# Kernel tuning notes

Measured on AMD Instinct MI355X. Metric: run time of the kernel, lower is better.

Reference implementation:

```python
import jax, jax.numpy as jnp
import numpy as np
from jax.scipy.special import gammaln

EPS = 1e-8
N_SAMPLES = 2 ** 17
ATTACK_FULL_SIZE = 2048
CPD = 16
N_RES = 16
EXPR = 2
N_OSC = 2
N_GAUSS = 8
N_EVENTS = 4
FRAMES = 128
DEF_FRAMES = 128
N_LEVELS = 11  # log2(ATTACK_FULL_SIZE)


def unit_norm(x, axis=-1):
    return x / (jnp.linalg.norm(x, axis=axis, keepdims=True) + EPS)


def fft_convolve(a, b):
    # zero-pad to 2n to avoid circular wraparound, multiply spectra, crop to n
    n = a.shape[-1]
    fa = jnp.fft.rfft(a, n=2 * n, axis=-1)
    fb = jnp.fft.rfft(b, n=2 * n, axis=-1)
    return jnp.fft.irfft(fa * fb, n=2 * n, axis=-1)[..., :n]


def upsample_with_holes(x, size):
    # zero-insertion upsampling: place frames at stride `factor`
    factor = size // x.shape[-1]
    out = jnp.zeros(x.shape[:-1] + (size,), x.dtype)
    return out.at[..., ::factor].set(x)


def interpolate_last_axis(x, size):
    # linear interpolation, align_corners=False semantics (torch F.interpolate)
    n = x.shape[-1]
    scale = n / size
    src = jnp.clip((jnp.arange(size) + 0.5) * scale - 0.5, 0.0, n - 1.0)
    lo = jnp.floor(src).astype(jnp.int32)
    hi = jnp.minimum(lo + 1, n - 1)
    w = (src - lo).astype(x.dtype)
    return x[..., lo] * (1.0 - w) + x[..., hi] * w


def ensure_last_axis_length(x, size):
    n = x.shape[-1]
    if n == size:
        return x
    if n > size:
        return x[..., :size]
    return jnp.pad(x, [(0, 0)] * (x.ndim - 1) + [(0, size - n)])


def sparse_softmax(x):
    # hard one-hot forward, softmax straight-through backward
    sm = jax.nn.softmax(x, axis=-1)
    hard = jax.nn.one_hot(jnp.argmax(x, axis=-1), x.shape[-1], dtype=x.dtype)
    return hard + sm - jax.lax.stop_gradient(sm)


def hierarchical_dirac(p):
    # p: (..., L, 2) binary choices per level -> one-hot dirac of length 2**L
    sel = sparse_softmax(p)
    sig = sel[..., 0, :]
    for i in range(1, p.shape[-2]):
        sig = (sig[..., :, None] * sel[..., i, :][..., None, :]).reshape(*sig.shape[:-1], -1)
    return sig


def gamma_pdf(mean, std, n_elements):
    # gamma pdf on support (eps, 1], parameterized by mean/std
    t = jnp.linspace(EPS, 1.0, n_elements)
    k = (mean / (std + EPS)) ** 2
    rate = mean / (std ** 2 + EPS)
    k = k[..., None]
    rate = rate[..., None]
    logp = k * jnp.log(rate + EPS) + (k - 1.0) * jnp.log(t) - rate * t - gammaln(k)
    return jnp.exp(logp)


def damped_harmonic_oscillator(time, mass, damping, tension, x0):
    # underdamped closed-form solution, v0 = 0
    omega0_sq = tension / mass
    gamma = damping / (2.0 * mass)
    omega = jnp.sqrt(omega0_sq - gamma ** 2)
    A = x0
    B = gamma * x0 / omega
    return jnp.exp(-gamma * time) * (A * jnp.cos(omega * time) + B * jnp.sin(omega * time))


def dho_block(damping, mass, tension, disp, amps, tmod=None, scaling=None):
    time = jnp.linspace(0.0, 10.0, N_SAMPLES).reshape(1, 1, 1, N_SAMPLES)
    t = tension[..., None]  # (N_OSC, N_RES, EXPR, 1)
    if tmod is not None:
        t = t + tmod[0] * scaling  # broadcast -> (N_OSC, N_RES, EXPR, N_SAMPLES)
    x = damped_harmonic_oscillator(
        time,
        jax.nn.sigmoid(mass[..., None]) * 2.0,
        jax.nn.sigmoid(damping[..., None]) * 30.0,
        10.0 ** t,
        disp[..., None],
    )
    x = (x * amps).sum(axis=0)  # sum over oscillators
    return x.reshape(1, 1, N_RES, EXPR, N_SAMPLES)


def attack_envelopes(means, stds, amps, pos, overall_amp):
    m, s, a = jnp.abs(means), jnp.abs(stds), jnp.abs(amps)
    p = hierarchical_dirac(pos)  # (1,1,CPD,NG,2048)
    x = gamma_pdf(m, s, ATTACK_FULL_SIZE) * a[..., None]
    x = fft_convolve(x, p)
    x = x.sum(axis=2)  # (1,1,NG,2048)
    x = unit_norm(x)
    x = x * overall_amp[..., None]  # broadcast -> (1,1,CPD,NG,2048)
    x = x.sum(axis=-2)  # (1,1,CPD,2048)
    return x.reshape(CPD, ATTACK_FULL_SIZE)


def _forward(control_signal, deformations, ae_means, ae_stds, ae_amps, ae_pos,
             ae_overall_amp, dho_damping, dho_mass, dho_tension, dho_disp, dho_amp,
             influences, stack_mix, router, layer_mix, gains, attack_noise):
    b, ne, cpd, frames = control_signal.shape
    # --- DampedHarmonicOscillatorStack ---
    o1 = dho_block(dho_damping[0], dho_mass[0], dho_tension[0], dho_disp[0], dho_amp[0])
    o2 = dho_block(dho_damping[1], dho_mass[1], dho_tension[1], dho_disp[1], dho_amp[1], o1, influences[0])
    o3 = dho_block(dho_damping[2], dho_mass[2], dho_tension[2], dho_disp[2], dho_amp[2], o2, influences[1])
    res = (jnp.stack([o1, o2, o3], axis=-1) * jax.nn.softmax(stack_mix, axis=-1)).sum(axis=-1)
    res = unit_norm(res)
    # --- AttackEnvelopes ---
    ae = attack_envelopes(ae_means, ae_stds, ae_amps, ae_pos, ae_overall_amp)
    # --- execute_layer ---
    routed = jnp.einsum('becf,cr->berf', control_signal, router)
    before = routed
    res = unit_norm(res)  # execute_layer normalizes again
    routed = upsample_with_holes(routed.reshape(b, ne, N_RES, 1, frames), N_SAMPLES)
    # ae.shape[-1] == window_size, so materialize_attack_envelopes just multiplies noise
    impulse = ensure_last_axis_length(ae * attack_noise, N_SAMPLES).reshape(1, 1, cpd, 1, N_SAMPLES)
    routed = fft_convolve(impulse, routed)  # (1,ne,N_RES,1,S)
    cs = routed.reshape(1, ne, cpd, N_SAMPLES).sum(axis=1, keepdims=True)
    conv = fft_convolve(routed, res)  # (1,ne,N_RES,EXPR,S)
    base = jnp.zeros_like(deformations).at[:, :, 0:1, :].set(1.0)
    d = jax.nn.softmax(base + deformations, axis=-2)
    d = interpolate_last_axis(d.reshape(b, 1, 1, EXPR, -1), N_SAMPLES)
    x = (d * conv).sum(axis=-2)  # (1,ne,N_RES,S)
    mixes = jax.nn.softmax(layer_mix.reshape(1, 1, N_RES, 1, 1, 2), axis=-1)
    stacked = jnp.stack([routed, x.reshape(routed.shape)], axis=-1)
    x = (mixes * stacked).sum(axis=-1)
    x = x.reshape(1, 1, N_RES, -1)
    summed = jnp.tanh(x * jnp.abs(gains.reshape(1, 1, N_RES, 1)))
    summed = summed.sum(axis=-2, keepdims=True)
    return summed, before, cs


def setup_inputs() -> dict:
    key = jax.random.key(0)
    ks = jax.random.split(key, 20)
    u = lambda k, shape, lo, hi: jax.random.uniform(k, shape, jnp.float32, lo, hi)
    inp = {}
    inp['control_signal'] = jax.random.uniform(ks[0], (1, N_EVENTS, CPD, FRAMES), jnp.float32)
    inp['deformations'] = jax.random.normal(ks[1], (1, 1, EXPR, DEF_FRAMES), jnp.float32)
    inp['ae_means'] = u(ks[2], (1, 1, CPD, N_GAUSS), -6.0, 6.0)
    inp['ae_stds'] = u(ks[3], (1, 1, CPD, N_GAUSS), 0.5, 6.0)
    inp['ae_amps'] = u(ks[4], (1, 1, CPD, N_GAUSS), -6.0, 6.0)
    inp['ae_pos'] = u(ks[5], (1, 1, CPD, N_GAUSS, N_LEVELS, 2), -1.0, 1.0)
    inp['ae_overall_amp'] = u(ks[6], (1, 1, CPD, 1), -1.0, 1.0)
    inp['dho_damping'] = u(ks[7], (3, N_OSC, N_RES, EXPR), 0.5, 1.5)
    inp['dho_mass'] = u(ks[8], (3, N_OSC, N_RES, EXPR), -2.0, 2.0)
    inp['dho_tension'] = u(ks[9], (3, N_OSC, N_RES, EXPR), 4.0, 9.0)
    inp['dho_disp'] = u(ks[10], (3, N_OSC, N_RES, EXPR), -1.0, 2.0)
    inp['dho_amp'] = u(ks[11], (3, N_OSC, N_RES, EXPR, 1), -1.0, 1.0)
    inp['influences'] = u(ks[12], (2, N_OSC, N_RES, EXPR, 1), -0.01, 0.01)
    inp['stack_mix'] = u(ks[13], (1, 1, N_RES, EXPR, 1, 3), -1.0, 1.0)
    router = u(ks[14], (CPD, N_RES), -1.0, 1.0)
    mask = (jax.random.uniform(ks[15], (CPD, N_RES)) < 0.1).astype(jnp.float32)
    inp['router'] = router * mask
    inp['layer_mix'] = u(ks[16], (N_RES, 2), -1.0, 1.0)
    inp['gains'] = u(ks[17], (N_RES, 1), 0.01, 1.1)
    inp['attack_noise'] = u(ks[18], (CPD, ATTACK_FULL_SIZE), -1.0, 1.0)
    return inp


def reference(control_signal, deformations, ae_means, ae_stds, ae_amps, ae_pos,
              ae_overall_amp, dho_damping, dho_mass, dho_tension, dho_disp, dho_amp,
              influences, stack_mix, router, layer_mix, gains, attack_noise):
    return _forward(control_signal, deformations, ae_means, ae_stds, ae_amps, ae_pos,
                    ae_overall_amp, dho_damping, dho_mass, dho_tension, dho_disp, dho_amp,
                    influences, stack_mix, router, layer_mix, gains, attack_noise)
```

## Files before the change

kernel.cpp:

```cpp
#include <hip/hip_runtime.h>
#include <math.h>

#define NS 131072
#define EPSF 1e-8f

#define OFF_IMP    8388608u
#define OFF_VG     8421376u
#define OFF_DW     8437760u
#define OFF_FV     8568832u
#define OFF_NORM   8577024u
#define OFF_MIX0   8577064u
#define OFF_MIX1   8577080u
#define OFF_GABS   8577096u
#define OFF_PART   8578560u
#define OFF_GSSP   8594944u
#define OFF_DHP    8595200u

#define AFRAG_USH  4194304u
#define ABF2_USH   4726784u
#define HB_USH     8388608u

typedef __attribute__((ext_vector_type(8))) short short8;
typedef __attribute__((ext_vector_type(4))) float floatx4;
typedef __attribute__((ext_vector_type(4))) unsigned short ushort4v;

#define INV2PI 0.15915494309189535f

__device__ __forceinline__ float sigmf(float x) { return 1.0f / (1.0f + expf(-x)); }

__device__ __forceinline__ unsigned short f2bf(float x) {
  unsigned u = __float_as_uint(x);
  unsigned r = (u + 0x7FFFu + ((u >> 16) & 1u)) >> 16;
  return (unsigned short)r;
}

__global__ __launch_bounds__(256) void k0_params(
    const float* __restrict__ ddmp, const float* __restrict__ dmas,
    const float* __restrict__ dten, const float* __restrict__ ddisp,
    const float* __restrict__ damp, const float* __restrict__ infl,
    const float* __restrict__ smix, float* __restrict__ wsf)
{
  int tid = threadIdx.x;
  int rx = tid >> 3, ent = tid & 7;
  int r = rx >> 1, x = rx & 1;
  float* g = wsf + OFF_DHP + rx * 40;
  if (ent < 6) {
    int bb = ent >> 1, o = ent & 1;
    int id = ((bb * 2 + o) * 16 + r) * 2 + x;
    float mass = 2.0f * sigmf(dmas[id]);
    float gam = 30.0f * sigmf(ddmp[id]) / (2.0f * mass);
    double W = exp((double)dten[id] * 2.302585092994046) / (double)mass;
    float x0v = ddisp[id];
    float ampv = damp[id];
    float infv = 0.f;
    if (bb == 1) infv = infl[(o * 16 + r) * 2 + x];
    if (bb == 2) infv = infl[((2 + o) * 16 + r) * 2 + x];
    g[0 + ent]  = -gam;
    g[6 + ent]  = ampv * x0v;
    g[12 + ent] = gam * ampv * x0v;
    g[18 + ent] = infv * 2.3025851f;
    if (bb == 0) {
      double om = sqrt(W - (double)gam * (double)gam);
      g[24 + o] = (float)((double)(gam * x0v * ampv) / om);
      g[26 + o] = (float)(om * 0.15915494309189535);
    } else {
      g[28 + ent - 2] = (float)W;
    }
    if (ent == 0) { g[32] = 0.f; g[36] = 0.f; g[37] = 0.f; g[38] = 0.f; g[39] = 0.f; }
  } else if (ent == 6) {
    float a0 = smix[rx * 3], a1 = smix[rx * 3 + 1], a2 = smix[rx * 3 + 2];
    float mm = fmaxf(a0, fmaxf(a1, a2));
    float e0 = expf(a0 - mm), e1 = expf(a1 - mm), e2 = expf(a2 - mm);
    float inv = 1.0f / (e0 + e1 + e2);
    g[33] = e0 * inv; g[34] = e1 * inv; g[35] = e2 * inv;
  }
}

__global__ __launch_bounds__(256) void k01_prep_dho(
    const float* __restrict__ csig, const float* __restrict__ deform,
    const float* __restrict__ smix_unused, const float* __restrict__ router,
    const float* __restrict__ lmix, const float* __restrict__ gains,
    const float* __restrict__ means, const float* __restrict__ stds,
    const float* __restrict__ amps, const float* __restrict__ pos,
    float* __restrict__ wsf, unsigned short* __restrict__ abf2,
    unsigned short* __restrict__ resb, float* __restrict__ partials,
    float* __restrict__ out)
{
  int tid = threadIdx.x;
  int bid = blockIdx.x;
  if (bid < 512) {
    int t = bid * 256 + tid;
    {
      float4 z = {0.f, 0.f, 0.f, 0.f};
      *(float4*)&out[(size_t)t * 4] = z;
    }
    {
      float src = (t + 0.5f) * (1.0f / 1024.0f) - 0.5f;
      src = fminf(fmaxf(src, 0.0f), 127.0f);
      int lo = (int)src;
      int hi = min(lo + 1, 127);
      float w = src - (float)lo;
      float c0l = 1.0f / (1.0f + expf(deform[128 + lo] - (1.0f + deform[lo])));
      float c0h = 1.0f / (1.0f + expf(deform[128 + hi] - (1.0f + deform[hi])));
      wsf[OFF_DW + t] = c0l * (1.0f - w) + c0h * w;
    }
    int mt = bid & 7, e = (bid >> 3) & 3, r = (bid >> 5) & 15;
    __shared__ float fvrow[128];
    if (tid < 128) {
      float s = 0.f;
      for (int c = 0; c < 16; ++c)
        s += csig[(e * 16 + c) * 128 + tid] * router[c * 16 + r];
      fvrow[tid] = s;
      if (mt == 0) {
        wsf[OFF_FV + (e * 16 + r) * 128 + tid] = s;
        out[524288 + (e * 16 + r) * 128 + tid] = s;
      }
    }
    __syncthreads();
    {
      int gid = bid * 256 + tid;
      int lane = gid & 63;
      int kt = (gid >> 6) & 3;
      int m = lane & 15, quad = lane >> 4;
      int base = mt * 16 + m - kt * 32 - quad * 8;
      short8 v;
#pragma unroll
      for (int j = 0; j < 8; ++j) {
        int f = base - j;
        unsigned short b = 0;
        if (f >= 0 && f < 128) b = f2bf(fvrow[f]);
        v[j] = (short)b;
      }
      *(short8*)&abf2[(size_t)gid * 8] = v;
    }
    if (bid == 0 && tid < 16) {
      int r2 = tid;
      float l0 = lmix[r2 * 2], l1 = lmix[r2 * 2 + 1];
      float mx = fmaxf(l0, l1);
      float e0 = expf(l0 - mx), e1 = expf(l1 - mx), inv = 1.0f / (e0 + e1);
      wsf[OFF_MIX0 + r2] = e0 * inv;
      wsf[OFF_MIX1 + r2] = e1 * inv;
      wsf[OFF_GABS + r2] = fabsf(gains[r2]);
    }
  } else if (bid < 576) {
    int gb = bid - 512;
    int g = gb >> 3;
    int i = (gb & 7) * 256 + tid;
    __shared__ float kS[16], rateS[16], logAS[16], aS[16];
    __shared__ int dS[16];
    __shared__ float red[4];
    if (tid < 16) {
      int c = tid, idx = c * 8 + g;
      double m = fabs((double)means[idx]);
      double s = fabs((double)stds[idx]);
      double k = m / (s + 1e-8); k = k * k;
      double rate = m / (s * s + 1e-8);
      double logA = k * log(rate + 1e-8) - lgamma(k);
      kS[c] = (float)k; rateS[c] = (float)rate; logAS[c] = (float)logA;
      aS[c] = fabsf(amps[idx]);
      int d = 0;
      for (int l = 0; l < 11; ++l) {
        float p0 = pos[(idx * 11 + l) * 2], p1 = pos[(idx * 11 + l) * 2 + 1];
        d = d * 2 + (p1 > p0 ? 1 : 0);
      }
      dS[c] = d;
    }
    __syncthreads();
    const float step = (float)((1.0 - 1e-8) / 2047.0);
    float v = 0.f;
    for (int c = 0; c < 16; ++c) {
      int mi = i - dS[c];
      if (mi >= 0) {
        float tm = 1e-8f + (float)mi * step;
        float lp = logAS[c] + (kS[c] - 1.0f) * __logf(tm) - rateS[c] * tm;
        v += aS[c] * __expf(lp);
      }
    }
    wsf[OFF_VG + g * 2048 + i] = v;
    float sumsq = v * v;
#pragma unroll
    for (int off = 32; off; off >>= 1) sumsq += __shfl_down(sumsq, off, 64);
    if ((tid & 63) == 0) red[tid >> 6] = sumsq;
    __syncthreads();
    if (tid == 0) wsf[OFF_GSSP + gb] = red[0] + red[1] + red[2] + red[3];
  } else {
    int b = bid - 576;
    int rx = b >> 8;
    int t0 = (b & 255) * 512 + tid * 2;
    __shared__ float pf[40];
    __shared__ float bred[4];
    if (tid < 40) pf[tid] = wsf[OFF_DHP + rx * 40 + tid];
    __syncthreads();
    float sqacc = 0.f;
    unsigned short h2[2];
#pragma unroll
    for (int u = 0; u < 2; ++u) {
      float ttf = (float)(t0 + u) * (10.0f / 131071.0f);
      float o1v = 0.f;
#pragma unroll
      for (int o = 0; o < 2; ++o) {
        float fr = pf[26 + o] * ttf;
        fr -= rintf(fr);
        float sn = __builtin_amdgcn_sinf(fr);
        float cn = __builtin_amdgcn_cosf(fr);
        float ex = __expf(pf[o] * ttf);
        o1v += ex * (pf[6 + o] * cn + pf[24 + o] * sn);
      }
      float prev = o1v, o2v = 0.f, o3v = 0.f;
#pragma unroll
      for (int blk = 1; blk < 3; ++blk) {
        float acc = 0.f;
#pragma unroll
        for (int oo = 0; oo < 2; ++oo) {
          int o = blk * 2 + oo;
          float ng = pf[o];
          float p10 = __expf(prev * pf[18 + o]);
          float rad = __builtin_fmaf(pf[28 + o - 2], p10, -(ng * ng));
          float om = __builtin_amdgcn_sqrtf(rad);
          float fr = (om * INV2PI) * ttf;
          fr -= rintf(fr);
          float sn = __builtin_amdgcn_sinf(fr);
          float cn = __builtin_amdgcn_cosf(fr);
          float Bp = pf[12 + o] * __builtin_amdgcn_rcpf(om);
          float ex = __expf(ng * ttf);
          acc += ex * (pf[6 + o] * cn + Bp * sn);
        }
        if (blk == 1) o2v = acc; else o3v = acc;
        prev = acc;
      }
      float rv = pf[33] * o1v + pf[34] * o2v + pf[35] * o3v;
      h2[u] = f2bf(rv);
      sqacc += rv * rv;
    }
    *(unsigned*)&resb[(size_t)rx * NS + t0] =
        (unsigned)h2[0] | ((unsigned)h2[1] << 16);
#pragma unroll
    for (int off = 32; off; off >>= 1) sqacc += __shfl_down(sqacc, off, 64);
    if ((tid & 63) == 0) bred[tid >> 6] = sqacc;
    __syncthreads();
    if (tid == 0)
      partials[rx * 512 + (b & 255)] = bred[0] + bred[1] + bred[2] + bred[3];
  }
}

__global__ __launch_bounds__(256) void kB_mid(
    const float* __restrict__ ovamp, const float* __restrict__ noise,
    float* __restrict__ wsf, unsigned short* __restrict__ abf)
{
  int bid = blockIdx.x;
  int tid = threadIdx.x;
  if (bid < 32) {
    int rx = bid;
    const float* partials = wsf + OFF_PART;
    __shared__ float red[4];
    float s = partials[rx * 512 + tid];
#pragma unroll
    for (int off = 32; off; off >>= 1) s += __shfl_down(s, off, 64);
    if ((tid & 63) == 0) red[tid >> 6] = s;
    __syncthreads();
    if (tid == 0) wsf[OFF_NORM + rx] = red[0] + red[1] + red[2] + red[3];
    return;
  }
  __shared__ float wS[8];
  if (tid < 8) {
    float g8 = 0.f;
#pragma unroll
    for (int u = 0; u < 8; ++u) g8 += wsf[OFF_GSSP + tid * 8 + u];
    wS[tid] = 1.0f / (sqrtf(g8) + EPSF);
  }
  __syncthreads();
  const float* vg = wsf + OFF_VG;
  if (bid < 160) {
    int idx0 = bid - 32;
    int c = idx0 >> 3;
    int i = (idx0 & 7) * 256 + tid;
    float S = 0.f;
#pragma unroll
    for (int g = 0; g < 8; ++g) S += vg[g * 2048 + i] * wS[g];
    wsf[OFF_IMP + c * 2048 + i] = ovamp[c] * S * noise[c * 2048 + i];
    return;
  }
  int gid = (bid - 160) * 256 + tid;
  if (gid >= 66560) return;
  int r = gid / (65 * 64);
  int rem = gid % (65 * 64);
  int sc = rem >> 6, lane = rem & 63;
  int m = lane & 15, quad = lane >> 4;
  int qp = (quad < 2) ? quad : quad - 4;
  int base = 32 * sc + m - 8 * qp;
  float oa = ovamp[r];
  short8 v;
#pragma unroll
  for (int j = 0; j < 8; ++j) {
    int idx = base - j;
    unsigned short b = 0;
    if (idx >= 0 && idx < 2048) {
      float S = 0.f;
#pragma unroll
      for (int g = 0; g < 8; ++g) S += vg[g * 2048 + idx] * wS[g];
      b = f2bf(oa * S * noise[r * 2048 + idx]);
    }
    v[j] = (short)b;
  }
  *(short8*)&abf[(size_t)gid * 8] = v;
}

__global__ __launch_bounds__(256) void k4_mfma(
    const unsigned short* __restrict__ resb, const unsigned short* __restrict__ abf,
    const float* __restrict__ wsf, unsigned short* __restrict__ Hb)
{
  int rx = blockIdx.y, r = rx >> 1;
  int n0 = blockIdx.x * 256;
  __shared__ __align__(16) unsigned short Xs[9280];
  int tid = threadIdx.x;
  for (int i = tid; i < 772; i += 256) {
    int q_rel = i >> 1, p8 = (i & 1) * 8;
    int q = n0 - 130 + q_rel;
    short8 v = {0, 0, 0, 0, 0, 0, 0, 0};
    if (q >= 0) v = *(const short8*)&resb[(size_t)rx * NS + q * 16 + p8];
    *(short8*)&Xs[q_rel * 24 + p8] = v;
  }
  __syncthreads();
  int lane = tid & 63, w = tid >> 6;
  int quad = lane >> 4, nl = lane & 15;
  float n1 = sqrtf(wsf[OFF_NORM + rx]);
  float s1 = 1.0f / (n1 + EPSF);
  float scale = s1 * (1.0f / (n1 * s1 + EPSF)) * wsf[OFF_MIX1 + r];
  const short8* af = (const short8*)(abf) + (size_t)r * 65 * 64 + lane;
  floatx4 acc0 = {0,0,0,0}, acc1 = {0,0,0,0}, acc2 = {0,0,0,0}, acc3 = {0,0,0,0};
  const char* xbase = (const char*)Xs + (size_t)(130 + w * 64 + nl - (quad >> 1)) * 48
                      + (quad & 1) * 16;
  short8 wbuf[25];
#pragma unroll
  for (int s = -24; s < 0; ++s)
    wbuf[s + 25] = *(const short8*)(xbase - 96 * s);
#pragma unroll
  for (int sc = 0; sc < 65; ++sc) {
    wbuf[sc % 25] = *(const short8*)(xbase - 96 * sc);
    short8 a = af[sc * 64];
    acc0 = __builtin_amdgcn_mfma_f32_16x16x32_bf16(a, wbuf[sc % 25],        acc0, 0, 0, 0);
    acc1 = __builtin_amdgcn_mfma_f32_16x16x32_bf16(a, wbuf[(sc + 17) % 25], acc1, 0, 0, 0);
    acc2 = __builtin_amdgcn_mfma_f32_16x16x32_bf16(a, wbuf[(sc + 9) % 25],  acc2, 0, 0, 0);
    acc3 = __builtin_amdgcn_mfma_f32_16x16x32_bf16(a, wbuf[(sc + 1) % 25],  acc3, 0, 0, 0);
  }
  unsigned short* hp = Hb + (size_t)rx * NS + 16 * (n0 + w * 64 + nl) + quad * 4;
  ushort4v h0, h1, h2, h3;
#pragma unroll
  for (int i = 0; i < 4; ++i) {
    h0[i] = f2bf(acc0[i] * scale);
    h1[i] = f2bf(acc1[i] * scale);
    h2[i] = f2bf(acc2[i] * scale);
    h3[i] = f2bf(acc3[i] * scale);
  }
  *(ushort4v*)(hp)       = h0;
  *(ushort4v*)(hp + 256) = h1;
  *(ushort4v*)(hp + 512) = h2;
  *(ushort4v*)(hp + 768) = h3;
}

#define HPAD 136
__global__ __launch_bounds__(256) void k6_mfma(
    const unsigned short* __restrict__ Hb, const float* __restrict__ imp,
    const unsigned short* __restrict__ abf2,
    const float* __restrict__ wsf, float* __restrict__ out)
{
  int r = blockIdx.y;
  int n0 = blockIdx.x * 32;
  int zz = blockIdx.z;
  int rm = r & 3, rq = r >> 2;
  int tid = threadIdx.x;
  int w = tid >> 6, lane = tid & 63;
  int wc = w & 1, wm = w >> 1;
  int quad = lane >> 4, n = lane & 15;
  int cl = wc * 16 + n;
  int col = n0 + cl;

  __shared__ float fvs[4][128];
  __shared__ __align__(16) unsigned short hs[2 * 32 * HPAD];
  for (int i = tid; i < 512; i += 256)
    fvs[i >> 7][i & 127] = wsf[OFF_FV + ((i >> 7) * 16 + r) * 128 + (i & 127)];
  {
    int rxs = tid >> 7, p = tid & 127;
    const unsigned short* src = Hb + (size_t)(2 * r + rxs) * NS + (size_t)p * 1024 + n0;
    unsigned short* dst = hs + rxs * 32 * HPAD + p;
#pragma unroll
    for (int b4 = 0; b4 < 4; ++b4) {
      short8 v = *(const short8*)(src + b4 * 8);
#pragma unroll
      for (int c = 0; c < 8; ++c)
        dst[(size_t)(b4 * 8 + c) * HPAD] = (unsigned short)v[c];
    }
  }
  __syncthreads();

  short8 bf0[4], bf1[4];
#pragma unroll
  for (int kt = 0; kt < 4; ++kt) {
    bf0[kt] = *(const short8*)&hs[(0 * 32 + cl) * HPAD + kt * 32 + quad * 8];
    bf1[kt] = *(const short8*)&hs[(1 * 32 + cl) * HPAD + kt * 32 + quad * 8];
  }

  float d0r[2][4];
  const float* dwg = wsf + OFF_DW;
#pragma unroll
  for (int mi = 0; mi < 2; ++mi)
#pragma unroll
    for (int i = 0; i < 4; ++i) {
      int q = (zz * 4 + wm * 2 + mi) * 16 + quad * 4 + i;
      d0r[mi][i] = dwg[q * 1024 + col];
    }

  float impA = imp[r * 2048 + col];
  float impB = imp[r * 2048 + 1024 + col];
  float mix0r = wsf[OFF_MIX0 + r];

  float tansum[2][4], csum[2][4];
#pragma unroll
  for (int mi = 0; mi < 2; ++mi)
#pragma unroll
    for (int i = 0; i < 4; ++i) { tansum[mi][i] = 0.f; csum[mi][i] = 0.f; }

  const short8* af = (const short8*)abf2;
  for (int e = 0; e < 4; ++e) {
    float ge = wsf[OFF_GABS + 4 * e + rq];
    const short8* afe = af + ((size_t)(r * 4 + e) * 32) * 64 + lane;
#pragma unroll
    for (int mi = 0; mi < 2; ++mi) {
      int mt = zz * 4 + wm * 2 + mi;
      floatx4 acc0 = {0, 0, 0, 0}, acc1 = {0, 0, 0, 0};
#pragma unroll
      for (int kt = 0; kt < 4; ++kt) {
        short8 a = afe[(mt * 4 + kt) * 64];
        acc0 = __builtin_amdgcn_mfma_f32_16x16x32_bf16(a, bf0[kt], acc0, 0, 0, 0);
        acc1 = __builtin_amdgcn_mfma_f32_16x16x32_bf16(a, bf1[kt], acc1, 0, 0, 0);
      }
#pragma unroll
      for (int i = 0; i < 4; ++i) {
        int q = mt * 16 + quad * 4 + i;
        float fq = fvs[e][q];
        float fqm = (q > 0) ? fvs[e][q - 1] : 0.f;
        float rsv = fq * impA + fqm * impB;
        csum[mi][i] += rsv;
        float d0 = d0r[mi][i];
        float conv = d0 * acc0[i] + (1.0f - d0) * acc1[i];
        float z = (mix0r * rsv + conv) * ge;
        float e2 = __expf(2.0f * z);
        tansum[mi][i] += 1.0f - 2.0f * __builtin_amdgcn_rcpf(e2 + 1.0f);
      }
    }
  }
#pragma unroll
  for (int mi = 0; mi < 2; ++mi)
#pragma unroll
    for (int i = 0; i < 4; ++i) {
      int q = (zz * 4 + wm * 2 + mi) * 16 + quad * 4 + i;
      atomicAdd(&out[(size_t)rm * NS + q * 1024 + col], tansum[mi][i]);
      out[532480 + (size_t)r * NS + q * 1024 + col] = csum[mi][i];
    }
}

extern "C" void kernel_launch(void* const* d_in, const int* in_sizes, int n_in,
                              void* d_out, int out_size, void* d_ws, size_t ws_size,
                              hipStream_t stream) {
  const float* csig   = (const float*)d_in[0];
  const float* deform = (const float*)d_in[1];
  const float* aem    = (const float*)d_in[2];
  const float* aes    = (const float*)d_in[3];
  const float* aea    = (const float*)d_in[4];
  const float* aep    = (const float*)d_in[5];
  const float* aeo    = (const float*)d_in[6];
  const float* ddmp   = (const float*)d_in[7];
  const float* dmas   = (const float*)d_in[8];
  const float* dten   = (const float*)d_in[9];
  const float* ddisp  = (const float*)d_in[10];
  const float* damp   = (const float*)d_in[11];
  const float* infl   = (const float*)d_in[12];
  const float* smix   = (const float*)d_in[13];
  const float* router = (const float*)d_in[14];
  const float* lmix   = (const float*)d_in[15];
  const float* gains  = (const float*)d_in[16];
  const float* anoise = (const float*)d_in[17];

  float*  wsf = (float*)d_ws;
  unsigned short* resb = (unsigned short*)d_ws;
  unsigned short* abf  = (unsigned short*)d_ws + AFRAG_USH;
  unsigned short* abf2 = (unsigned short*)d_ws + ABF2_USH;
  unsigned short* Hb   = (unsigned short*)d_ws + HB_USH;
  float*  out = (float*)d_out;

  k0_params<<<1, 256, 0, stream>>>(ddmp, dmas, dten, ddisp, damp, infl, smix, wsf);
  k01_prep_dho<<<8768, 256, 0, stream>>>(csig, deform, smix, router, lmix, gains,
                                         aem, aes, aea, aep, wsf, abf2, resb,
                                         wsf + OFF_PART, out);
  kB_mid<<<420, 256, 0, stream>>>(aeo, anoise, wsf, abf);
  k4_mfma<<<dim3(32, 32), 256, 0, stream>>>(resb, abf, wsf, Hb);
  k6_mfma<<<dim3(32, 16, 2), 256, 0, stream>>>(Hb, wsf + OFF_IMP, abf2, wsf, out);
}
```

Baseline: 164.4 us.

## Reduce over resonator groups inside k6 blocks instead of atomics; widen DHO per-thread work

k6 now gives each block one output channel and 16 columns, and it loops over the four resonators that feed that channel. The sum is kept in registers and written with a plain store, so the atomicAdd and the zeroing of the output in k01 are no longer needed. The B fragments are now read straight from global memory with strided 16-bit loads, replacing the transposed shared-memory staging. The DHO branch of k01 computes four samples per thread, which halves its block count, and the partial-norm reduction is adjusted to match. The strided scalar global loads for H could be slow and uncoalesced, and the grid of k6 becomes smaller.

```diff
diff --git a/kernel.cpp b/kernel.cpp
--- a/kernel.cpp
+++ b/kernel.cpp
@@ -91,10 +91,6 @@
   if (bid < 512) {
     int t = bid * 256 + tid;
     {
-      float4 z = {0.f, 0.f, 0.f, 0.f};
-      *(float4*)&out[(size_t)t * 4] = z;
-    }
-    {
       float src = (t + 0.5f) * (1.0f / 1024.0f) - 0.5f;
       src = fminf(fmaxf(src, 0.0f), 127.0f);
       int lo = (int)src;
@@ -185,16 +181,16 @@
     if (tid == 0) wsf[OFF_GSSP + gb] = red[0] + red[1] + red[2] + red[3];
   } else {
     int b = bid - 576;
-    int rx = b >> 8;
-    int t0 = (b & 255) * 512 + tid * 2;
+    int rx = b >> 7;
+    int t0 = (b & 127) * 1024 + tid * 4;
     __shared__ float pf[40];
     __shared__ float bred[4];
     if (tid < 40) pf[tid] = wsf[OFF_DHP + rx * 40 + tid];
     __syncthreads();
     float sqacc = 0.f;
-    unsigned short h2[2];
-#pragma unroll
-    for (int u = 0; u < 2; ++u) {
+    unsigned short h4[4];
+#pragma unroll
+    for (int u = 0; u < 4; ++u) {
       float ttf = (float)(t0 + u) * (10.0f / 131071.0f);
       float o1v = 0.f;
 #pragma unroll
@@ -229,17 +225,18 @@
         prev = acc;
       }
       float rv = pf[33] * o1v + pf[34] * o2v + pf[35] * o3v;
-      h2[u] = f2bf(rv);
+      h4[u] = f2bf(rv);
       sqacc += rv * rv;
     }
-    *(unsigned*)&resb[(size_t)rx * NS + t0] =
-        (unsigned)h2[0] | ((unsigned)h2[1] << 16);
+    ushort4v hv;
+    hv[0] = h4[0]; hv[1] = h4[1]; hv[2] = h4[2]; hv[3] = h4[3];
+    *(ushort4v*)&resb[(size_t)rx * NS + t0] = hv;
 #pragma unroll
     for (int off = 32; off; off >>= 1) sqacc += __shfl_down(sqacc, off, 64);
     if ((tid & 63) == 0) bred[tid >> 6] = sqacc;
     __syncthreads();
     if (tid == 0)
-      partials[rx * 512 + (b & 255)] = bred[0] + bred[1] + bred[2] + bred[3];
+      partials[rx * 512 + (b & 127)] = bred[0] + bred[1] + bred[2] + bred[3];
   }
 }
 
@@ -253,7 +250,7 @@
     int rx = bid;
     const float* partials = wsf + OFF_PART;
     __shared__ float red[4];
-    float s = partials[rx * 512 + tid];
+    float s = (tid < 128) ? partials[rx * 512 + tid] : 0.f;
 #pragma unroll
     for (int off = 32; off; off >>= 1) s += __shfl_down(s, off, 64);
     if ((tid & 63) == 0) red[tid >> 6] = s;
@@ -358,75 +355,60 @@
   *(ushort4v*)(hp + 768) = h3;
 }
 
-#define HPAD 136
 __global__ __launch_bounds__(256) void k6_mfma(
     const unsigned short* __restrict__ Hb, const float* __restrict__ imp,
     const unsigned short* __restrict__ abf2,
     const float* __restrict__ wsf, float* __restrict__ out)
 {
-  int r = blockIdx.y;
-  int n0 = blockIdx.x * 32;
+  int rm = blockIdx.y;
+  int n0 = blockIdx.x * 16;
   int zz = blockIdx.z;
-  int rm = r & 3, rq = r >> 2;
   int tid = threadIdx.x;
-  int w = tid >> 6, lane = tid & 63;
-  int wc = w & 1, wm = w >> 1;
+  int wm = tid >> 6, lane = tid & 63;
   int quad = lane >> 4, n = lane & 15;
-  int cl = wc * 16 + n;
-  int col = n0 + cl;
-
-  __shared__ float fvs[4][128];
-  __shared__ __align__(16) unsigned short hs[2 * 32 * HPAD];
-  for (int i = tid; i < 512; i += 256)
-    fvs[i >> 7][i & 127] = wsf[OFF_FV + ((i >> 7) * 16 + r) * 128 + (i & 127)];
-  {
-    int rxs = tid >> 7, p = tid & 127;
-    const unsigned short* src = Hb + (size_t)(2 * r + rxs) * NS + (size_t)p * 1024 + n0;
-    unsigned short* dst = hs + rxs * 32 * HPAD + p;
-#pragma unroll
-    for (int b4 = 0; b4 < 4; ++b4) {
-      short8 v = *(const short8*)(src + b4 * 8);
-#pragma unroll
-      for (int c = 0; c < 8; ++c)
-        dst[(size_t)(b4 * 8 + c) * HPAD] = (unsigned short)v[c];
-    }
+  int col = n0 + n;
+  int mt = zz * 4 + wm;
+
+  __shared__ float fvs2[4][4][128];
+  for (int i = tid; i < 2048; i += 256) {
+    int rq = i >> 9, e = (i >> 7) & 3, q = i & 127;
+    fvs2[rq][e][q] = wsf[OFF_FV + (e * 16 + rq * 4 + rm) * 128 + q];
   }
   __syncthreads();
 
-  short8 bf0[4], bf1[4];
-#pragma unroll
-  for (int kt = 0; kt < 4; ++kt) {
-    bf0[kt] = *(const short8*)&hs[(0 * 32 + cl) * HPAD + kt * 32 + quad * 8];
-    bf1[kt] = *(const short8*)&hs[(1 * 32 + cl) * HPAD + kt * 32 + quad * 8];
-  }
-
-  float d0r[2][4];
+  float d0r[4];
   const float* dwg = wsf + OFF_DW;
 #pragma unroll
-  for (int mi = 0; mi < 2; ++mi)
-#pragma unroll
-    for (int i = 0; i < 4; ++i) {
-      int q = (zz * 4 + wm * 2 + mi) * 16 + quad * 4 + i;
-      d0r[mi][i] = dwg[q * 1024 + col];
-    }
-
-  float impA = imp[r * 2048 + col];
-  float impB = imp[r * 2048 + 1024 + col];
-  float mix0r = wsf[OFF_MIX0 + r];
-
-  float tansum[2][4], csum[2][4];
-#pragma unroll
-  for (int mi = 0; mi < 2; ++mi)
-#pragma unroll
-    for (int i = 0; i < 4; ++i) { tansum[mi][i] = 0.f; csum[mi][i] = 0.f; }
-
+  for (int i = 0; i < 4; ++i) {
+    int q = mt * 16 + quad * 4 + i;
+    d0r[i] = dwg[q * 1024 + col];
+  }
+
+  float tansum[4] = {0.f, 0.f, 0.f, 0.f};
   const short8* af = (const short8*)abf2;
-  for (int e = 0; e < 4; ++e) {
-    float ge = wsf[OFF_GABS + 4 * e + rq];
-    const short8* afe = af + ((size_t)(r * 4 + e) * 32) * 64 + lane;
-#pragma unroll
-    for (int mi = 0; mi < 2; ++mi) {
-      int mt = zz * 4 + wm * 2 + mi;
+
+  for (int rq = 0; rq < 4; ++rq) {
+    int r = rq * 4 + rm;
+    short8 bf0[4], bf1[4];
+    const unsigned short* H0 = Hb + (size_t)(2 * r) * NS + col;
+    const unsigned short* H1 = Hb + (size_t)(2 * r + 1) * NS + col;
+#pragma unroll
+    for (int kt = 0; kt < 4; ++kt) {
+#pragma unroll
+      for (int j = 0; j < 8; ++j) {
+        int p = kt * 32 + quad * 8 + j;
+        bf0[kt][j] = (short)H0[(size_t)p * 1024];
+        bf1[kt][j] = (short)H1[(size_t)p * 1024];
+      }
+    }
+    float impA = imp[r * 2048 + col];
+    float impB = imp[r * 2048 + 1024 + col];
+    float mix0r = wsf[OFF_MIX0 + r];
+    float csum[4] = {0.f, 0.f, 0.f, 0.f};
+
+    for (int e = 0; e < 4; ++e) {
+      float ge = wsf[OFF_GABS + 4 * e + rq];
+      const short8* afe = af + ((size_t)(r * 4 + e) * 32) * 64 + lane;
       floatx4 acc0 = {0, 0, 0, 0}, acc1 = {0, 0, 0, 0};
 #pragma unroll
       for (int kt = 0; kt < 4; ++kt) {
@@ -437,26 +419,28 @@
 #pragma unroll
       for (int i = 0; i < 4; ++i) {
         int q = mt * 16 + quad * 4 + i;
-        float fq = fvs[e][q];
-        float fqm = (q > 0) ? fvs[e][q - 1] : 0.f;
+        float fq = fvs2[rq][e][q];
+        float fqm = (q > 0) ? fvs2[rq][e][q - 1] : 0.f;
         float rsv = fq * impA + fqm * impB;
-        csum[mi][i] += rsv;
-        float d0 = d0r[mi][i];
+        csum[i] += rsv;
+        float d0 = d0r[i];
         float conv = d0 * acc0[i] + (1.0f - d0) * acc1[i];
         float z = (mix0r * rsv + conv) * ge;
         float e2 = __expf(2.0f * z);
-        tansum[mi][i] += 1.0f - 2.0f * __builtin_amdgcn_rcpf(e2 + 1.0f);
-      }
-    }
-  }
-#pragma unroll
-  for (int mi = 0; mi < 2; ++mi)
+        tansum[i] += 1.0f - 2.0f * __builtin_amdgcn_rcpf(e2 + 1.0f);
+      }
+    }
 #pragma unroll
     for (int i = 0; i < 4; ++i) {
-      int q = (zz * 4 + wm * 2 + mi) * 16 + quad * 4 + i;
-      atomicAdd(&out[(size_t)rm * NS + q * 1024 + col], tansum[mi][i]);
-      out[532480 + (size_t)r * NS + q * 1024 + col] = csum[mi][i];
-    }
+      int q = mt * 16 + quad * 4 + i;
+      out[532480 + (size_t)r * NS + q * 1024 + col] = csum[i];
+    }
+  }
+#pragma unroll
+  for (int i = 0; i < 4; ++i) {
+    int q = mt * 16 + quad * 4 + i;
+    out[(size_t)rm * NS + q * 1024 + col] = tansum[i];
+  }
 }
 
 extern "C" void kernel_launch(void* const* d_in, const int* in_sizes, int n_in,
@@ -489,10 +473,10 @@
   float*  out = (float*)d_out;
 
   k0_params<<<1, 256, 0, stream>>>(ddmp, dmas, dten, ddisp, damp, infl, smix, wsf);
-  k01_prep_dho<<<8768, 256, 0, stream>>>(csig, deform, smix, router, lmix, gains,
+  k01_prep_dho<<<4672, 256, 0, stream>>>(csig, deform, smix, router, lmix, gains,
                                          aem, aes, aea, aep, wsf, abf2, resb,
                                          wsf + OFF_PART, out);
   kB_mid<<<420, 256, 0, stream>>>(aeo, anoise, wsf, abf);
   k4_mfma<<<dim3(32, 32), 256, 0, stream>>>(resb, abf, wsf, Hb);
-  k6_mfma<<<dim3(32, 16, 2), 256, 0, stream>>>(Hb, wsf + OFF_IMP, abf2, wsf, out);
-}
+  k6_mfma<<<dim3(64, 4, 2), 256, 0, stream>>>(Hb, wsf + OFF_IMP, abf2, wsf, out);
+}
```

Result: no change. 163.0 us (-0.9%).
